# Kernel tuning notes

Measured on AMD Instinct MI355X. Metric: run time of the kernel, lower is better.

Reference implementation:

```python
import jax, jax.numpy as jnp
import numpy as np
import math

H = 8          # num_heads
DH = 16        # dim_head
DEPTH = 1
LAMBDA_INIT = 0.8 - 0.6 * math.exp(-0.3 * DEPTH)
LN_EPS = 1e-5


def setup_inputs() -> dict:
    key = jax.random.key(0)
    ks = jax.random.split(key, 12)
    dim = 256
    inner = 2 * H * DH  # 256
    b, n = 2, 2048
    s = lambda fan_in: 1.0 / math.sqrt(fan_in)
    return {
        "x": jax.random.normal(ks[0], (b, n, dim), jnp.float32),
        "Wq": jax.random.normal(ks[1], (dim, inner), jnp.float32) * s(dim),
        "Wkv": jax.random.normal(ks[2], (dim, 2 * inner), jnp.float32) * s(dim),
        "Wout": jax.random.normal(ks[3], (inner, dim), jnp.float32) * s(inner),
        "bout": jnp.zeros((dim,), jnp.float32),
        "Wg": jax.random.normal(ks[4], (dim, inner), jnp.float32) * s(dim),
        "bg": jnp.ones((inner,), jnp.float32),
        "lq1": jax.random.normal(ks[5], (DH,), jnp.float32) * 0.1,
        "lk1": jax.random.normal(ks[6], (DH,), jnp.float32) * 0.1,
        "lq2": jax.random.normal(ks[7], (DH,), jnp.float32) * 0.1,
        "lk2": jax.random.normal(ks[8], (DH,), jnp.float32) * 0.1,
        "ln_gamma": jnp.ones((2 * DH,), jnp.float32),
        "ln_beta": jnp.zeros((2 * DH,), jnp.float32),
    }


def reference(x, Wq, Wkv, Wout, bout, Wg, bg, lq1, lk1, lq2, lk2, ln_gamma, ln_beta):
    b, n, dim = x.shape
    scale = DH ** (-0.5)

    q = x @ Wq                                   # [b, n, 2*H*DH]
    kv = x @ Wkv                                 # [b, n, 4*H*DH]
    k, v = jnp.split(kv, 2, axis=-1)

    # doubled heads for q, k; normal heads with width 2*DH for v
    q = q.reshape(b, n, 2 * H, DH).transpose(0, 2, 1, 3) * scale  # [b, 2H, n, DH]
    k = k.reshape(b, n, 2 * H, DH).transpose(0, 2, 1, 3)          # [b, 2H, n, DH]
    v = v.reshape(b, n, H, 2 * DH).transpose(0, 2, 1, 3)          # [b, H, n, 2DH]

    dots = jnp.einsum('bhid,bhjd->bhij', q, k)   # [b, 2H, n, n]
    attn = jax.nn.softmax(dots, axis=-1)

    lam1 = jnp.exp(jnp.sum(lq1 * lk1))
    lam2 = jnp.exp(jnp.sum(lq2 * lk2))
    lam = lam1 - lam2 + LAMBDA_INIT

    attn = attn.reshape(b, H, 2, n, n)
    attn = attn[:, :, 0] - lam * attn[:, :, 1]   # [b, H, n, n]

    out = jnp.einsum('bhij,bhjd->bhid', attn, v)  # [b, H, n, 2DH]

    # LayerNorm over last dim (2*DH)
    mu = jnp.mean(out, axis=-1, keepdims=True)
    var = jnp.var(out, axis=-1, keepdims=True)
    out = (out - mu) * jax.lax.rsqrt(var + LN_EPS) * ln_gamma + ln_beta

    out = out * (1.0 - LAMBDA_INIT)
    out = out.transpose(0, 2, 1, 3).reshape(b, n, H * 2 * DH)  # [b, n, inner]

    gates = x @ Wg + bg
    out = out * jax.nn.sigmoid(gates)
    return out @ Wout + bout
```

## Files before the change

### kernel.cpp

```cpp
#include <hip/hip_runtime.h>
#include <hip/hip_bf16.h>

#define LAMBDA_INIT_F 0.35550906759096927f
#define ONE_MINUS_LI  0.64449093240903073f
#define QSCALE 0.36067376022224085f

typedef unsigned short u16;
typedef unsigned int   u32;
typedef short s4v  __attribute__((ext_vector_type(4)));
typedef short s8v  __attribute__((ext_vector_type(8)));
typedef u32   u32x4 __attribute__((ext_vector_type(4)));
typedef float f16v __attribute__((ext_vector_type(16)));

__device__ __forceinline__ u16 f2bf(float f) {
    __hip_bfloat16 h = __float2bfloat16(f);
    return *reinterpret_cast<u16*>(&h);
}
__device__ __forceinline__ u32 pk2bf(float lo, float hi) {
    return (u32)f2bf(lo) | ((u32)f2bf(hi) << 16);
}
union U4S8 { u32 u[4]; s8v s; };
__device__ __forceinline__ s8v mks8(u32 a, u32 b, u32 c, u32 d) {
    U4S8 x; x.u[0]=a; x.u[1]=b; x.u[2]=c; x.u[3]=d; return x.s;
}

__device__ __forceinline__ float fexp2(float x) {
#if __has_builtin(__builtin_amdgcn_exp2f)
    return __builtin_amdgcn_exp2f(x);
#else
    float r; asm volatile("v_exp_f32 %0, %1\n\ts_nop 1" : "=v"(r) : "v"(x)); return r;
#endif
}

#define MFMA16(a,b,c) __builtin_amdgcn_mfma_f32_32x32x16_bf16((a),(b),(c),0,0,0)

__device__ __forceinline__ void plswap2(u32& a, u32& b) {
    auto r = __builtin_amdgcn_permlane32_swap(a, b, false, false);
    a = r[0]; b = r[1];
}

__global__ __launch_bounds__(256) void prep_kernel(
    const float* __restrict__ Wq, const float* __restrict__ Wkv,
    const float* __restrict__ Wg, const float* __restrict__ Wout,
    const float* __restrict__ x,
    u16* __restrict__ WT, u16* __restrict__ xbf)
{
    const int bid = blockIdx.x;
    const int tid = threadIdx.x;

    if (bid >= 80) {
        const int r0 = (bid - 80) * 64;
        const float2* src = (const float2*)(x + (size_t)r0 * 256);
        u32* dst = (u32*)(xbf + (size_t)r0 * 256);
        for (int idx = tid; idx < 64 * 128; idx += 256) {
            float2 v = src[idx];
            dst[idx] = pk2bf(v.x, v.y);
        }
        return;
    }

    __shared__ u16 tile[16 * 258];
    const int n0g = bid * 16;
    const float* src; int cols; int ncol0;
    if      (n0g < 256)  { src = Wq;   cols = 256; ncol0 = n0g; }
    else if (n0g < 768)  { src = Wkv;  cols = 512; ncol0 = n0g - 256; }
    else if (n0g < 1024) { src = Wg;   cols = 256; ncol0 = n0g - 768; }
    else                 { src = Wout; cols = 256; ncol0 = n0g - 1024; }

    const float* srow = src + (size_t)tid * cols + ncol0;
#pragma unroll
    for (int j = 0; j < 8; ++j) {
        const float2 v = *(const float2*)(srow + 2*j);
        tile[(2*j + 0) * 258 + tid] = f2bf(v.x);
        tile[(2*j + 1) * 258 + tid] = f2bf(v.y);
    }
    __syncthreads();

    const u32* t32 = (const u32*)tile;
    const int nn = tid >> 4, part = tid & 15;
    u32* dst = (u32*)WT + (size_t)(n0g + nn) * 128 + part * 8;
    const u32* s2 = t32 + nn * 129 + part * 8;
#pragma unroll
    for (int j = 0; j < 8; ++j) dst[j] = s2[j];
}

__global__ __launch_bounds__(256) void proj_kernel(
    const u16* __restrict__ x, const u16* __restrict__ WT,
    const float* __restrict__ bg,
    u16* __restrict__ Qb, u16* __restrict__ Kb,
    u16* __restrict__ Vb, float* __restrict__ Gb)
{
    const int bid = blockIdx.x;
    const int nt = bid & 15, mt = bid >> 4;
    const int tid = threadIdx.x, w = tid >> 6, lane = tid & 63;
    const int l31 = lane & 31, hh = lane >> 5;
    const int m0 = mt * 128 + w * 32;
    const int n0 = nt * 64;

    const u16* xr  = x  + (size_t)(m0 + l31) * 256 + 8*hh;
    const u16* br0 = WT + (size_t)(n0 + l31) * 256 + 8*hh;
    const u16* br1 = WT + (size_t)(n0 + 32 + l31) * 256 + 8*hh;

    f16v a0, a1;
#pragma unroll
    for (int r = 0; r < 16; ++r) { a0[r] = 0.f; a1[r] = 0.f; }

#pragma unroll
    for (int ks = 0; ks < 16; ++ks) {
        s8v xa = *(const s8v*)(xr  + ks*16);
        s8v w0 = *(const s8v*)(br0 + ks*16);
        s8v w1 = *(const s8v*)(br1 + ks*16);
        a0 = MFMA16(xa, w0, a0);
        a1 = MFMA16(xa, w1, a1);
    }

    const int cat = nt >> 2;
#pragma unroll
    for (int ns = 0; ns < 2; ++ns) {
        const f16v& acc = ns ? a1 : a0;
        const int n = nt * 64 + ns * 32 + l31;
#pragma unroll
        for (int r = 0; r < 16; ++r) {
            const int il = (r & 3) + 8*(r >> 2) + 4*hh;
            const int R = m0 + il;
            const int b = R >> 11, i = R & 2047;
            const float v = acc[r];
            if (cat == 0) {
                const int h = n >> 4, d = n & 15;
                Qb[((size_t)(b*16 + h) * 2048 + i) * 16 + d] = f2bf(v * QSCALE);
            } else if (cat == 1) {
                const int nk = n - 256, h = nk >> 4, d = nk & 15;
                Kb[((size_t)(b*16 + h) * 2048 + i) * 16 + d] = f2bf(v);
            } else if (cat == 2) {
                const int nv = n - 512, hv = nv >> 5, d2 = nv & 31;
                Vb[((size_t)(b*8 + hv) * 2048 + i) * 32 + d2] = f2bf(v);
            } else {
                const int gcol = n - 768;
                const float t = v + bg[gcol];
                Gb[(size_t)R * 256 + gcol] = 1.0f / (1.0f + __expf(-t));
            }
        }
    }
}

__global__ __launch_bounds__(512, 8) void attn_kernel(
    const u16* __restrict__ Q, const u16* __restrict__ K,
    const u16* __restrict__ V, const float* __restrict__ G,
    const float* __restrict__ lq1, const float* __restrict__ lk1,
    const float* __restrict__ lq2, const float* __restrict__ lk2,
    const float* __restrict__ gamma, const float* __restrict__ beta,
    u16* __restrict__ A)
{
    __shared__ float smemf[8960];
    u16* st  = (u16*)smemf;
    u32* stu = (u32*)smemf;

    const int bid = blockIdx.x;
    const int itile = bid & 63;
    const int combo = bid >> 6;
    const int ho = combo & 7, b = combo >> 3;
    const int i0 = itile * 32;

    const int tid = threadIdx.x, w = tid >> 6, lane = tid & 63;
    const int l31 = lane & 31, hh = lane >> 5;
    const int s = w & 1, jq = w >> 1;

    const u16* Vg = V + (size_t)(b*8 + ho) * 2048 * 32;
    const u16* Qg = Q + ((size_t)(b*16 + 2*ho + s) * 2048 + (i0 + l31)) * 16;
    const s8v qf = *(const s8v*)(Qg + 8*hh);

    const int qp = tid >> 7;
    const int pid = tid & 127;
    const int ksub = pid >> 6, krow = (pid >> 1) & 31, kseg = pid & 1;
    const u32* kgp = (const u32*)(K + (size_t)(b*16 + 2*ho + ksub) * 2048 * 16)
                     + (size_t)qp * 4096 + krow * 8 + kseg * 4;
    const int vj = pid >> 2, vseg = pid & 3;
    const u32* vgp = (const u32*)Vg + (size_t)qp * 8192 + vj * 16 + vseg * 4;

    const int kw_off = qp*1120 + ksub*288 + krow*9 + kseg*4;
    const int vw_u16 = qp*2240 + 1152 + vj;
    const int vd0 = vseg * 8;
    const int kr_off = jq*1120 + s*288 + l31*9 + 4*hh;
    const int vr_off = jq*1120 + 576 + l31*17;

    f16v oacc;
#pragma unroll
    for (int r = 0; r < 16; ++r) oacc[r] = 0.f;
    float la0 = 0.f, la1 = 0.f;

    {
        u32 k0 = kgp[0], k1 = kgp[1], k2 = kgp[2], k3 = kgp[3];
        u32 v0 = vgp[0], v1 = vgp[1], v2 = vgp[2], v3 = vgp[3];
        u32* kd = stu + kw_off;
        kd[0]=k0; kd[1]=k1; kd[2]=k2; kd[3]=k3;
        u16* vd = st + vw_u16;
        vd[(vd0+0)*34] = (u16)(v0 & 0xffff); vd[(vd0+1)*34] = (u16)(v0 >> 16);
        vd[(vd0+2)*34] = (u16)(v1 & 0xffff); vd[(vd0+3)*34] = (u16)(v1 >> 16);
        vd[(vd0+4)*34] = (u16)(v2 & 0xffff); vd[(vd0+5)*34] = (u16)(v2 >> 16);
        vd[(vd0+6)*34] = (u16)(v3 & 0xffff); vd[(vd0+7)*34] = (u16)(v3 >> 16);
    }

    for (int t = 0; t < 16; ++t) {
        __syncthreads();
        const int p = t & 1, pn = 1 - p;
        const int tt = (t + 1) & 15;

        const u32* kp = kgp + (size_t)tt * 256;
        u32 nk0=kp[0], nk1=kp[1], nk2=kp[2], nk3=kp[3];
        const u32* vp = vgp + (size_t)tt * 512;
        u32 nv0=vp[0], nv1=vp[1], nv2=vp[2], nv3=vp[3];

        const u32* kb2 = stu + p*4480 + kr_off;
        const u32* vb2 = stu + p*4480 + vr_off;

        f16v sc;
#pragma unroll
        for (int r = 0; r < 16; ++r) sc[r] = 0.f;
        {
            s8v kf = mks8(kb2[0], kb2[1], kb2[2], kb2[3]);
            sc = MFMA16(kf, qf, sc);
        }
        float pv[16];
#pragma unroll
        for (int r = 0; r < 16; ++r) pv[r] = fexp2(sc[r]);
        la0 += pv[0];  la0 += pv[1];  la0 += pv[2];  la0 += pv[3];
        la1 += pv[4];  la1 += pv[5];  la1 += pv[6];  la1 += pv[7];
        la0 += pv[8];  la0 += pv[9];  la0 += pv[10]; la0 += pv[11];
        la1 += pv[12]; la1 += pv[13]; la1 += pv[14]; la1 += pv[15];

        u32 wv[8];
#pragma unroll
        for (int i = 0; i < 8; ++i)
            wv[i] = __builtin_amdgcn_perm(__float_as_uint(pv[2*i+1]),
                                          __float_as_uint(pv[2*i+0]), 0x07060302);
        plswap2(wv[0], wv[2]); plswap2(wv[1], wv[3]);
        {
            s8v pf0 = mks8(wv[0], wv[1], wv[2], wv[3]);
            s8v vf0 = mks8(vb2[4*hh+0], vb2[4*hh+1], vb2[4*hh+2], vb2[4*hh+3]);
            oacc = MFMA16(pf0, vf0, oacc);
        }
        plswap2(wv[4], wv[6]); plswap2(wv[5], wv[7]);
        {
            s8v pf1 = mks8(wv[4], wv[5], wv[6], wv[7]);
            s8v vf1 = mks8(vb2[8+4*hh+0], vb2[8+4*hh+1], vb2[8+4*hh+2], vb2[8+4*hh+3]);
            oacc = MFMA16(pf1, vf1, oacc);
        }

        {
            u32* kd = stu + pn*4480 + kw_off;
            kd[0]=nk0; kd[1]=nk1; kd[2]=nk2; kd[3]=nk3;
            u16* vd = st + pn*8960 + vw_u16;
            vd[(vd0+0)*34] = (u16)(nv0 & 0xffff); vd[(vd0+1)*34] = (u16)(nv0 >> 16);
            vd[(vd0+2)*34] = (u16)(nv1 & 0xffff); vd[(vd0+3)*34] = (u16)(nv1 >> 16);
            vd[(vd0+4)*34] = (u16)(nv2 & 0xffff); vd[(vd0+5)*34] = (u16)(nv2 >> 16);
            vd[(vd0+6)*34] = (u16)(nv3 & 0xffff); vd[(vd0+7)*34] = (u16)(nv3 >> 16);
        }
    }
    const float lacc = la0 + la1;

    __syncthreads();
    float ltot = lacc + __shfl_xor(lacc, 32);
    float* ob = smemf + w * 1056;
#pragma unroll
    for (int r = 0; r < 16; ++r) {
        const int il = (r & 3) + 8*(r >> 2) + 4*hh;
        ob[il*33 + l31] = oacc[r];
    }
    if (lane < 32) smemf[8448 + w*32 + l31] = ltot;
    __syncthreads();

    if (tid < 128) {
        const int ii = tid >> 2, sub = tid & 3, d0 = sub * 8;
        float l1 = 0.f, l2 = 0.f;
#pragma unroll
        for (int q = 0; q < 4; ++q) {
            l1 += smemf[8448 + (2*q + 0)*32 + ii];
            l2 += smemf[8448 + (2*q + 1)*32 + ii];
        }

        float sA = 0.f, sB = 0.f;
#pragma unroll
        for (int d = 0; d < 16; ++d) {
            sA += lq1[d] * lk1[d];
            sB += lq2[d] * lk2[d];
        }
        const float lam = __expf(sA) - __expf(sB) + LAMBDA_INIT_F;
        const float c1 = 1.f / l1, c2 = lam / l2;

        float od[8]; float mu = 0.f;
#pragma unroll
        for (int dd = 0; dd < 8; ++dd) {
            const int d = d0 + dd;
            float o1 = 0.f, o2 = 0.f;
#pragma unroll
            for (int q = 0; q < 4; ++q) {
                o1 += smemf[(2*q + 0)*1056 + ii*33 + d];
                o2 += smemf[(2*q + 1)*1056 + ii*33 + d];
            }
            od[dd] = o1 * c1 - o2 * c2;
            mu += od[dd];
        }
        mu += __shfl_xor(mu, 1); mu += __shfl_xor(mu, 2);
        mu *= (1.f / 32.f);
        float var = 0.f;
#pragma unroll
        for (int dd = 0; dd < 8; ++dd) { const float t2 = od[dd] - mu; var += t2 * t2; }
        var += __shfl_xor(var, 1); var += __shfl_xor(var, 2);
        var *= (1.f / 32.f);
        const float rs = rsqrtf(var + 1e-5f);

        const int R = b*2048 + i0 + ii;
        const float* Gr = G + (size_t)R * 256 + ho*32 + d0;
        const float4 g0 = *(const float4*)(Gr);
        const float4 g1 = *(const float4*)(Gr + 4);
        const float gg[8] = { g0.x, g0.y, g0.z, g0.w, g1.x, g1.y, g1.z, g1.w };
        float vals[8];
#pragma unroll
        for (int dd = 0; dd < 8; ++dd) {
            const float val = (od[dd] - mu)*rs*gamma[d0 + dd] + beta[d0 + dd];
            vals[dd] = val * ONE_MINUS_LI * gg[dd];
        }
        u32x4 pk;
        pk[0] = pk2bf(vals[0], vals[1]);
        pk[1] = pk2bf(vals[2], vals[3]);
        pk[2] = pk2bf(vals[4], vals[5]);
        pk[3] = pk2bf(vals[6], vals[7]);
        *reinterpret_cast<u32x4*>(A + (size_t)R * 256 + ho*32 + d0) = pk;
    }
}

__global__ __launch_bounds__(512) void out_kernel(
    const u16* __restrict__ Abf, const u16* __restrict__ WT,
    const float* __restrict__ bout, float* __restrict__ out)
{
    __shared__ float cs[4][32 * 33];

    const int bid = blockIdx.x;
    const int nt = bid & 3, mt = bid >> 2;
    const int tid = threadIdx.x, w = tid >> 6, lane = tid & 63;
    const int l31 = lane & 31, hh = lane >> 5;
    const int t = w >> 1, kh = w & 1;
    const int m0 = mt * 64 + (t & 1) * 32;
    const int n0 = nt * 64 + (t >> 1) * 32;

    const u16* ar = Abf + (size_t)(m0 + l31) * 256 + kh*128 + 8*hh;
    const u16* br = WT + (size_t)(1024 + n0 + l31) * 256 + kh*128 + 8*hh;

    f16v acc;
#pragma unroll
    for (int r = 0; r < 16; ++r) acc[r] = 0.f;

#pragma unroll
    for (int ks = 0; ks < 8; ++ks) {
        s8v aa = *(const s8v*)(ar + ks*16);
        s8v ba = *(const s8v*)(br + ks*16);
        acc = MFMA16(aa, ba, acc);
    }

    if (kh == 0) {
#pragma unroll
        for (int r = 0; r < 16; ++r) {
            const int il = (r & 3) + 8*(r >> 2) + 4*hh;
            cs[t][il*33 + l31] = acc[r];
        }
    }
    __syncthreads();
    if (kh == 1) {
        const float bv = bout[n0 + l31];
#pragma unroll
        for (int r = 0; r < 16; ++r) {
            const int il = (r & 3) + 8*(r >> 2) + 4*hh;
            const int m = m0 + il;
            out[(size_t)m * 256 + n0 + l31] = acc[r] + cs[t][il*33 + l31] + bv;
        }
    }
}

extern "C" void kernel_launch(void* const* d_in, const int* in_sizes, int n_in,
                              void* d_out, int out_size, void* d_ws, size_t ws_size,
                              hipStream_t stream) {
    const float* x    = (const float*)d_in[0];
    const float* Wq   = (const float*)d_in[1];
    const float* Wkv  = (const float*)d_in[2];
    const float* Wout = (const float*)d_in[3];
    const float* bout = (const float*)d_in[4];
    const float* Wg   = (const float*)d_in[5];
    const float* bg   = (const float*)d_in[6];
    const float* lq1  = (const float*)d_in[7];
    const float* lk1  = (const float*)d_in[8];
    const float* lq2  = (const float*)d_in[9];
    const float* lk2  = (const float*)d_in[10];
    const float* lng  = (const float*)d_in[11];
    const float* lnb  = (const float*)d_in[12];

    u16*   WT  = (u16*)d_ws;
    u16*   xbf = WT + 327680;
    u16*   Qb  = xbf + 1048576;
    u16*   Kb  = Qb + 1048576;
    u16*   Vb  = Kb + 1048576;
    float* Gb  = (float*)(Vb + 1048576);
    u16*   Abf = (u16*)(Gb + 1048576);

    hipLaunchKernelGGL(prep_kernel, dim3(144), dim3(256), 0, stream,
                       Wq, Wkv, Wg, Wout, x, WT, xbf);
    hipLaunchKernelGGL(proj_kernel, dim3(512), dim3(256), 0, stream,
                       xbf, WT, bg, Qb, Kb, Vb, Gb);
    hipLaunchKernelGGL(attn_kernel, dim3(1024), dim3(512), 0, stream,
                       Qb, Kb, Vb, Gb, lq1, lk1, lq2, lk2, lng, lnb, Abf);
    hipLaunchKernelGGL(out_kernel, dim3(256), dim3(512), 0, stream,
                       Abf, WT, bout, (float*)d_out);
}
```

Measured before the change: 141.5 us.

## Split projection GEMM K dimension across wave pairs with LDS reduction

The projection kernel now runs 512 threads per block. Each output tile is computed by two waves that each handle half of the K=256 reduction, and the partial sums are combined through shared memory before the scattered Q/K/V/G stores. This halves the serial MFMA and load chain per wave and doubles the waves available to hide memory latency, at the cost of an LDS round-trip and a block barrier. The x-to-bf16 conversion in the prep kernel also switches to float4 loads.

```diff
diff --git a/kernel.cpp b/kernel.cpp
--- a/kernel.cpp
+++ b/kernel.cpp
@@ -50,11 +50,12 @@
 
     if (bid >= 80) {
         const int r0 = (bid - 80) * 64;
-        const float2* src = (const float2*)(x + (size_t)r0 * 256);
+        const float4* src = (const float4*)(x + (size_t)r0 * 256);
         u32* dst = (u32*)(xbf + (size_t)r0 * 256);
-        for (int idx = tid; idx < 64 * 128; idx += 256) {
-            float2 v = src[idx];
-            dst[idx] = pk2bf(v.x, v.y);
+        for (int idx = tid; idx < 64 * 64; idx += 256) {
+            float4 v = src[idx];
+            dst[2*idx + 0] = pk2bf(v.x, v.y);
+            dst[2*idx + 1] = pk2bf(v.z, v.w);
         }
         return;
     }
@@ -84,29 +85,32 @@
     for (int j = 0; j < 8; ++j) dst[j] = s2[j];
 }
 
-__global__ __launch_bounds__(256) void proj_kernel(
+__global__ __launch_bounds__(512, 4) void proj_kernel(
     const u16* __restrict__ x, const u16* __restrict__ WT,
     const float* __restrict__ bg,
     u16* __restrict__ Qb, u16* __restrict__ Kb,
     u16* __restrict__ Vb, float* __restrict__ Gb)
 {
+    __shared__ float cs[4][2][32 * 33];
+
     const int bid = blockIdx.x;
     const int nt = bid & 15, mt = bid >> 4;
     const int tid = threadIdx.x, w = tid >> 6, lane = tid & 63;
     const int l31 = lane & 31, hh = lane >> 5;
-    const int m0 = mt * 128 + w * 32;
+    const int t = w >> 1, kh = w & 1;
+    const int m0 = mt * 128 + t * 32;
     const int n0 = nt * 64;
 
-    const u16* xr  = x  + (size_t)(m0 + l31) * 256 + 8*hh;
-    const u16* br0 = WT + (size_t)(n0 + l31) * 256 + 8*hh;
-    const u16* br1 = WT + (size_t)(n0 + 32 + l31) * 256 + 8*hh;
+    const u16* xr  = x  + (size_t)(m0 + l31) * 256 + kh*128 + 8*hh;
+    const u16* br0 = WT + (size_t)(n0 + l31) * 256 + kh*128 + 8*hh;
+    const u16* br1 = WT + (size_t)(n0 + 32 + l31) * 256 + kh*128 + 8*hh;
 
     f16v a0, a1;
 #pragma unroll
     for (int r = 0; r < 16; ++r) { a0[r] = 0.f; a1[r] = 0.f; }
 
 #pragma unroll
-    for (int ks = 0; ks < 16; ++ks) {
+    for (int ks = 0; ks < 8; ++ks) {
         s8v xa = *(const s8v*)(xr  + ks*16);
         s8v w0 = *(const s8v*)(br0 + ks*16);
         s8v w1 = *(const s8v*)(br1 + ks*16);
@@ -114,30 +118,44 @@
         a1 = MFMA16(xa, w1, a1);
     }
 
-    const int cat = nt >> 2;
-#pragma unroll
-    for (int ns = 0; ns < 2; ++ns) {
-        const f16v& acc = ns ? a1 : a0;
-        const int n = nt * 64 + ns * 32 + l31;
-#pragma unroll
-        for (int r = 0; r < 16; ++r) {
-            const int il = (r & 3) + 8*(r >> 2) + 4*hh;
-            const int R = m0 + il;
-            const int b = R >> 11, i = R & 2047;
-            const float v = acc[r];
-            if (cat == 0) {
-                const int h = n >> 4, d = n & 15;
-                Qb[((size_t)(b*16 + h) * 2048 + i) * 16 + d] = f2bf(v * QSCALE);
-            } else if (cat == 1) {
-                const int nk = n - 256, h = nk >> 4, d = nk & 15;
-                Kb[((size_t)(b*16 + h) * 2048 + i) * 16 + d] = f2bf(v);
-            } else if (cat == 2) {
-                const int nv = n - 512, hv = nv >> 5, d2 = nv & 31;
-                Vb[((size_t)(b*8 + hv) * 2048 + i) * 32 + d2] = f2bf(v);
-            } else {
-                const int gcol = n - 768;
-                const float t = v + bg[gcol];
-                Gb[(size_t)R * 256 + gcol] = 1.0f / (1.0f + __expf(-t));
+    if (kh == 0) {
+#pragma unroll
+        for (int ns = 0; ns < 2; ++ns) {
+            const f16v& acc = ns ? a1 : a0;
+#pragma unroll
+            for (int r = 0; r < 16; ++r) {
+                const int il = (r & 3) + 8*(r >> 2) + 4*hh;
+                cs[t][ns][il*33 + l31] = acc[r];
+            }
+        }
+    }
+    __syncthreads();
+    if (kh == 1) {
+        const int cat = nt >> 2;
+#pragma unroll
+        for (int ns = 0; ns < 2; ++ns) {
+            const f16v& acc = ns ? a1 : a0;
+            const int n = nt * 64 + ns * 32 + l31;
+#pragma unroll
+            for (int r = 0; r < 16; ++r) {
+                const int il = (r & 3) + 8*(r >> 2) + 4*hh;
+                const int R = m0 + il;
+                const int b = R >> 11, i = R & 2047;
+                const float v = acc[r] + cs[t][ns][il*33 + l31];
+                if (cat == 0) {
+                    const int h = n >> 4, d = n & 15;
+                    Qb[((size_t)(b*16 + h) * 2048 + i) * 16 + d] = f2bf(v * QSCALE);
+                } else if (cat == 1) {
+                    const int nk = n - 256, h = nk >> 4, d = nk & 15;
+                    Kb[((size_t)(b*16 + h) * 2048 + i) * 16 + d] = f2bf(v);
+                } else if (cat == 2) {
+                    const int nv = n - 512, hv = nv >> 5, d2 = nv & 31;
+                    Vb[((size_t)(b*8 + hv) * 2048 + i) * 32 + d2] = f2bf(v);
+                } else {
+                    const int gcol = n - 768;
+                    const float tg = v + bg[gcol];
+                    Gb[(size_t)R * 256 + gcol] = 1.0f / (1.0f + __expf(-tg));
+                }
             }
         }
     }
@@ -403,7 +421,7 @@
 
     hipLaunchKernelGGL(prep_kernel, dim3(144), dim3(256), 0, stream,
                        Wq, Wkv, Wg, Wout, x, WT, xbf);
-    hipLaunchKernelGGL(proj_kernel, dim3(512), dim3(256), 0, stream,
+    hipLaunchKernelGGL(proj_kernel, dim3(512), dim3(512), 0, stream,
                        xbf, WT, bg, Qb, Kb, Vb, Gb);
     hipLaunchKernelGGL(attn_kernel, dim3(1024), dim3(512), 0, stream,
                        Qb, Kb, Vb, Gb, lq1, lk1, lq2, lk2, lng, lnb, Abf);
```

After: 143.0 us. No clear change (+1.1%).
